# Kernel optimization log

Hardware: AMD Instinct MI355X
Metric: run time of the kernel (lower is better)

## Reference

```python
import jax, jax.numpy as jnp
import numpy as np


def setup_inputs() -> dict:
    key = jax.random.key(0)
    k1, k2, k3 = jax.random.split(key, 3)
    B, S, D_IN, D_OUT = 4, 2048, 4096, 4096
    x = jax.random.normal(k1, (B, S, D_IN), dtype=jnp.float32)
    weight = jax.random.normal(k2, (D_OUT, D_IN), dtype=jnp.float32) * 0.02
    bias = jax.random.normal(k3, (D_OUT,), dtype=jnp.float32) * 0.02
    return {"x": x, "weight": weight, "bias": bias}


def reference(x, weight, bias):
    # Column L1 norms over the output dim (torch.norm(w, p=1, dim=0)) -> [in_features]
    column_norms = jnp.abs(weight).sum(axis=0)
    q = jnp.quantile(column_norms, jnp.array([0.05, 0.95], dtype=column_norms.dtype))
    lower, upper = q[0], q[1]
    # NOTE: mask naming follows the source; 'outlier_columns' is actually the middle band.
    outlier_columns = (column_norms > lower) & (column_norms < upper)  # [in]
    binarized = ~outlier_columns  # columns that get rescaled (mask is inverted in source)

    # Row-wise abs-mean over the 'binarized' columns, detached. Shape [out, 1].
    n_bin = binarized.sum().astype(weight.dtype)
    scale = (jnp.abs(weight) * binarized[None, :]).sum(axis=-1, keepdims=True) / n_bin
    scale = jax.lax.stop_gradient(scale)

    # The STE sign assignment in the source is overwritten by w * scale, so the
    # effective binarized-column value is weight * scale (not sign(weight) * scale).
    w_bin = jnp.where(binarized[None, :], weight * scale, weight)  # [out, in]

    # F.linear(x, w_bin, bias)
    out = jnp.einsum('bsd,od->bso', x, w_bin) + bias
    return out
```

## Files before the change

kernel.cpp:

```cpp
#include <hip/hip_runtime.h>
#include <hip/hip_bf16.h>

typedef unsigned short u16;
typedef __bf16 bf16x8 __attribute__((ext_vector_type(8)));
typedef float f32x4 __attribute__((ext_vector_type(4)));
typedef __attribute__((address_space(1))) void* gp1_t;
typedef __attribute__((address_space(3))) void* lp3_t;

#define D_IN   4096
#define D_OUT  4096
#define M_ROWS 8192

#define OFF_NORMS  0u
#define OFF_QVALS  16384u
#define OFF_XB     573696u
#define OFF_WB     67682560u

static __device__ __forceinline__ u16 f2bf(float f) {
    __hip_bfloat16 h = __float2bfloat16(f);
    u16 u; __builtin_memcpy(&u, &h, 2);
    return u;
}

__global__ __launch_bounds__(256) void k1_cast_colnorm(const float* __restrict__ x,
                                                       const float* __restrict__ W,
                                                       u16* __restrict__ xb,
                                                       float* __restrict__ norms) {
    const int b = blockIdx.x;
    if (b < 512) {
        const int j  = (b & 15) * 256 + threadIdx.x;
        const int r0 = (b >> 4) * 128;
        float s = 0.f;
        #pragma unroll 4
        for (int r = 0; r < 128; ++r) s += fabsf(W[(size_t)(r0 + r) * D_IN + j]);
        atomicAdd(&norms[j], s);
    } else {
        const size_t i4 = (size_t)(b - 512) * 256 + threadIdx.x;
        const float4 v = ((const float4*)x)[i4];
        ushort4 r;
        r.x = f2bf(v.x); r.y = f2bf(v.y); r.z = f2bf(v.z); r.w = f2bf(v.w);
        ((ushort4*)xb)[i4] = r;
    }
}

__global__ void rank_select(const float* __restrict__ norms, float* __restrict__ qvals) {
    __shared__ float sn[D_IN];
    const int tid = threadIdx.x;
    for (int i = tid; i < D_IN; i += 256) sn[i] = norms[i];
    __syncthreads();
    const int j = blockIdx.x * 256 + tid;
    const float vj = sn[j];
    int r = 0;
    #pragma unroll 8
    for (int i = 0; i < D_IN; ++i) {
        const float vi = sn[i];
        r += (vi < vj) || (vi == vj && i < j);
    }
    if      (r == 204)  qvals[0] = vj;
    else if (r == 205)  qvals[1] = vj;
    else if (r == 3890) qvals[2] = vj;
    else if (r == 3891) qvals[3] = vj;
}

__global__ __launch_bounds__(256) void k3_scale_wbin(const float* __restrict__ W,
                                                     const float* __restrict__ norms,
                                                     const float* __restrict__ qvals,
                                                     u16* __restrict__ wb) {
    __shared__ float red[8];
    const int o = blockIdx.x, t = threadIdx.x;
    const int wave = t >> 6, lane = t & 63;
    const float lower = qvals[0] + 0.75f * (qvals[1] - qvals[0]);
    const float upper = qvals[2] + 0.25f * (qvals[3] - qvals[2]);
    const float4* row4 = (const float4*)(W + (size_t)o * D_IN);
    const float4* n4   = (const float4*)norms;

    float4 wv[4];
    int binbits[4];
    float cnt = 0.f, sum = 0.f;
    #pragma unroll
    for (int it = 0; it < 4; ++it) {
        const int c = it * 256 + t;
        wv[it] = row4[c];
        const float4 nv = n4[c];
        const bool b0 = !(nv.x > lower && nv.x < upper);
        const bool b1 = !(nv.y > lower && nv.y < upper);
        const bool b2 = !(nv.z > lower && nv.z < upper);
        const bool b3 = !(nv.w > lower && nv.w < upper);
        binbits[it] = (b0 ? 1 : 0) | (b1 ? 2 : 0) | (b2 ? 4 : 0) | (b3 ? 8 : 0);
        cnt += (float)(b0 + b1 + b2 + b3);
        sum += (b0 ? fabsf(wv[it].x) : 0.f) + (b1 ? fabsf(wv[it].y) : 0.f)
             + (b2 ? fabsf(wv[it].z) : 0.f) + (b3 ? fabsf(wv[it].w) : 0.f);
    }
    #pragma unroll
    for (int off = 32; off > 0; off >>= 1) {
        cnt += __shfl_down(cnt, off, 64);
        sum += __shfl_down(sum, off, 64);
    }
    if (lane == 0) { red[wave] = cnt; red[4 + wave] = sum; }
    __syncthreads();
    const float nbin = red[0] + red[1] + red[2] + red[3];
    const float ssum = red[4] + red[5] + red[6] + red[7];
    const float sc = ssum / nbin;

    ushort4* out = (ushort4*)(wb + (size_t)o * D_IN);
    #pragma unroll
    for (int it = 0; it < 4; ++it) {
        const int c = it * 256 + t;
        const int bb = binbits[it];
        ushort4 r;
        r.x = f2bf((bb & 1) ? wv[it].x * sc : wv[it].x);
        r.y = f2bf((bb & 2) ? wv[it].y * sc : wv[it].y);
        r.z = f2bf((bb & 4) ? wv[it].z * sc : wv[it].z);
        r.w = f2bf((bb & 8) ? wv[it].w * sc : wv[it].w);
        out[c] = r;
    }
}


#define BAR() do { asm volatile("" ::: "memory"); __builtin_amdgcn_s_barrier(); \
                   asm volatile("" ::: "memory"); } while (0)

#define LDA(buf, kh, mf) \
    (*(const bf16x8*)(smA + (buf)*32768 + (kh)*16384 + wr*8192 + (mf)*1024 + lane_rd))
#define LDB(buf, kh, nf) \
    (*(const bf16x8*)(smB + (buf)*32768 + (kh)*16384 + wc*4096 + (nf)*1024 + lane_rd))

#define STAGE_A(buf, kh, t) do { \
    char* l_ = smA + (buf)*32768 + (kh)*16384 + wofs; \
    __builtin_amdgcn_global_load_lds((gp1_t)(srcA0 + (t)*128 + (kh)*64), (lp3_t)l_, 16, 0, 0); \
    __builtin_amdgcn_global_load_lds((gp1_t)(srcA1 + (t)*128 + (kh)*64), (lp3_t)(l_ + 8192), 16, 0, 0); \
} while (0)

#define STAGE_B(buf, kh, t) do { \
    char* l_ = smB + (buf)*32768 + (kh)*16384 + wofs; \
    __builtin_amdgcn_global_load_lds((gp1_t)(srcB0 + (t)*128 + (kh)*64), (lp3_t)l_, 16, 0, 0); \
    __builtin_amdgcn_global_load_lds((gp1_t)(srcB1 + (t)*128 + (kh)*64), (lp3_t)(l_ + 8192), 16, 0, 0); \
} while (0)

#define MFMA __builtin_amdgcn_mfma_f32_16x16x32_bf16

#define PHASE(buf, kh, mg, RB, ST, VM) do { \
    bf16x8 a0_, a1_, a2_, a3_; \
    if (RB) { \
        bfr0 = LDB(buf, kh, 0); bfr1 = LDB(buf, kh, 1); \
        bfr2 = LDB(buf, kh, 2); bfr3 = LDB(buf, kh, 3); \
    } \
    a0_ = LDA(buf, kh, (mg)*4 + 0); \
    a1_ = LDA(buf, kh, (mg)*4 + 1); \
    a2_ = LDA(buf, kh, (mg)*4 + 2); \
    a3_ = LDA(buf, kh, (mg)*4 + 3); \
    ST; \
    if (VM) { asm volatile("s_waitcnt vmcnt(4)" ::: "memory"); } \
    BAR(); \
    asm volatile("s_waitcnt lgkmcnt(0)" ::: "memory"); \
    __builtin_amdgcn_sched_barrier(0); \
    __builtin_amdgcn_s_setprio(1); \
    acc[(mg)*4+0][0] = MFMA(a0_, bfr0, acc[(mg)*4+0][0], 0, 0, 0); \
    acc[(mg)*4+0][1] = MFMA(a0_, bfr1, acc[(mg)*4+0][1], 0, 0, 0); \
    acc[(mg)*4+0][2] = MFMA(a0_, bfr2, acc[(mg)*4+0][2], 0, 0, 0); \
    acc[(mg)*4+0][3] = MFMA(a0_, bfr3, acc[(mg)*4+0][3], 0, 0, 0); \
    acc[(mg)*4+1][0] = MFMA(a1_, bfr0, acc[(mg)*4+1][0], 0, 0, 0); \
    acc[(mg)*4+1][1] = MFMA(a1_, bfr1, acc[(mg)*4+1][1], 0, 0, 0); \
    acc[(mg)*4+1][2] = MFMA(a1_, bfr2, acc[(mg)*4+1][2], 0, 0, 0); \
    acc[(mg)*4+1][3] = MFMA(a1_, bfr3, acc[(mg)*4+1][3], 0, 0, 0); \
    acc[(mg)*4+2][0] = MFMA(a2_, bfr0, acc[(mg)*4+2][0], 0, 0, 0); \
    acc[(mg)*4+2][1] = MFMA(a2_, bfr1, acc[(mg)*4+2][1], 0, 0, 0); \
    acc[(mg)*4+2][2] = MFMA(a2_, bfr2, acc[(mg)*4+2][2], 0, 0, 0); \
    acc[(mg)*4+2][3] = MFMA(a2_, bfr3, acc[(mg)*4+2][3], 0, 0, 0); \
    acc[(mg)*4+3][0] = MFMA(a3_, bfr0, acc[(mg)*4+3][0], 0, 0, 0); \
    acc[(mg)*4+3][1] = MFMA(a3_, bfr1, acc[(mg)*4+3][1], 0, 0, 0); \
    acc[(mg)*4+3][2] = MFMA(a3_, bfr2, acc[(mg)*4+3][2], 0, 0, 0); \
    acc[(mg)*4+3][3] = MFMA(a3_, bfr3, acc[(mg)*4+3][3], 0, 0, 0); \
    __builtin_amdgcn_s_setprio(0); \
    BAR(); \
} while (0)

__global__ __launch_bounds__(512, 2) void gemm8(const u16* __restrict__ A, const u16* __restrict__ B,
                                                const float* __restrict__ bias, float* __restrict__ C) {
    __shared__ u16 sA[2][2][256 * 32];
    __shared__ u16 sB[2][2][256 * 32];
    char* const smA = (char*)&sA[0][0][0];
    char* const smB = (char*)&sB[0][0][0];

    const int tid  = threadIdx.x;
    const int wave = tid >> 6, lane = tid & 63;
    const int wr = wave >> 2, wc = wave & 3;
    const int r15 = lane & 15, q = lane >> 4;
    const int wofs = wave * 1024;

    const int swz = ((int)blockIdx.x & 7) * 64 + ((int)blockIdx.x >> 3);
    const int by = swz >> 4, bx = swz & 15;
    const int m0 = by * 256, n0 = bx * 256;

    const int lane_rd = (r15 * 64 + q * 16) ^ (((r15 >> 1) & 7) << 4);

    const int P0  = wofs + lane * 16;
    const int xv  = ((lane >> 3) & 7) << 4;
    const int lb0 = P0 ^ xv;
    const int lb1 = (P0 + 8192) ^ xv;
    const char* const gA = (const char*)(A + (size_t)m0 * D_IN);
    const char* const gB = (const char*)(B + (size_t)n0 * D_IN);
    const char* const srcA0 = gA + (size_t)(lb0 >> 6) * (D_IN * 2) + (lb0 & 63);
    const char* const srcA1 = gA + (size_t)(lb1 >> 6) * (D_IN * 2) + (lb1 & 63);
    const char* const srcB0 = gB + (size_t)(lb0 >> 6) * (D_IN * 2) + (lb0 & 63);
    const char* const srcB1 = gB + (size_t)(lb1 >> 6) * (D_IN * 2) + (lb1 & 63);

    f32x4 acc[8][4] = {};
    bf16x8 bfr0{}, bfr1{}, bfr2{}, bfr3{};

    STAGE_A(0, 0, 0); STAGE_B(0, 0, 0);
    STAGE_A(0, 1, 0); STAGE_B(0, 1, 0);
    STAGE_A(1, 0, 1); STAGE_B(1, 0, 1);
    asm volatile("s_waitcnt vmcnt(4)" ::: "memory");
    BAR();

    for (int i = 0; i < 32; ++i) {
        const int t1 = 2 * i + 1;
        const int t2 = (2 * i + 2 > 63) ? 63 : 2 * i + 2;
        const int t3 = (2 * i + 3 > 63) ? 63 : 2 * i + 3;
        PHASE(0, 0, 0, 1, STAGE_A(1, 1, t1), 0);
        PHASE(0, 0, 1, 0, STAGE_B(1, 1, t1), 0);
        PHASE(0, 1, 0, 1, STAGE_A(0, 0, t2), 0);
        PHASE(0, 1, 1, 0, STAGE_B(0, 0, t2), 1);
        PHASE(1, 0, 0, 1, STAGE_A(0, 1, t2), 0);
        PHASE(1, 0, 1, 0, STAGE_B(0, 1, t2), 0);
        PHASE(1, 1, 0, 1, STAGE_A(1, 0, t3), 0);
        PHASE(1, 1, 1, 0, STAGE_B(1, 0, t3), 1);
    }

    const int cm = q * 4;
    #pragma unroll
    for (int nf = 0; nf < 4; ++nf) {
        const int n = n0 + wc * 64 + nf * 16 + r15;
        const float bv = bias[n];
        #pragma unroll
        for (int mf = 0; mf < 8; ++mf) {
            const int mbase = m0 + wr * 128 + mf * 16 + cm;
            #pragma unroll
            for (int rr = 0; rr < 4; ++rr)
                C[(size_t)(mbase + rr) * D_OUT + n] = acc[mf][nf][rr] + bv;
        }
    }
    asm volatile("s_waitcnt vmcnt(0)" ::: "memory");
}

extern "C" void kernel_launch(void* const* d_in, const int* in_sizes, int n_in,
                              void* d_out, int out_size, void* d_ws, size_t ws_size,
                              hipStream_t stream) {
    const float* x    = (const float*)d_in[0];
    const float* W    = (const float*)d_in[1];
    const float* bias = (const float*)d_in[2];
    float* out = (float*)d_out;

    char* ws = (char*)d_ws;
    float* norms = (float*)(ws + OFF_NORMS);
    float* qvals = (float*)(ws + OFF_QVALS);
    u16*   xb    = (u16*)(ws + OFF_XB);
    u16*   wb    = (u16*)(ws + OFF_WB);

    hipMemsetAsync(norms, 0, D_IN * sizeof(float), stream);
    k1_cast_colnorm<<<512 + 32768, 256, 0, stream>>>(x, W, xb, norms);
    rank_select<<<16, 256, 0, stream>>>(norms, qvals);
    k3_scale_wbin<<<4096, 256, 0, stream>>>(W, norms, qvals, wb);
    gemm8<<<dim3(512), dim3(512), 0, stream>>>(xb, wb, bias, out);
}
```

Before: 647.9 us.

## Software-pipeline LDS fragment reads one phase ahead of MFMAs

```diff
diff --git a/kernel.cpp b/kernel.cpp
--- a/kernel.cpp
+++ b/kernel.cpp
@@ -125,52 +125,60 @@
 #define LDB(buf, kh, nf) \
     (*(const bf16x8*)(smB + (buf)*32768 + (kh)*16384 + wc*4096 + (nf)*1024 + lane_rd))
 
-#define STAGE_A(buf, kh, t) do { \
+#define STAGE_A(buf, kh, OFFV) do { \
     char* l_ = smA + (buf)*32768 + (kh)*16384 + wofs; \
-    __builtin_amdgcn_global_load_lds((gp1_t)(srcA0 + (t)*128 + (kh)*64), (lp3_t)l_, 16, 0, 0); \
-    __builtin_amdgcn_global_load_lds((gp1_t)(srcA1 + (t)*128 + (kh)*64), (lp3_t)(l_ + 8192), 16, 0, 0); \
-} while (0)
-
-#define STAGE_B(buf, kh, t) do { \
+    __builtin_amdgcn_global_load_lds((gp1_t)(srcA0 + (OFFV)), (lp3_t)l_, 16, 0, 0); \
+    __builtin_amdgcn_global_load_lds((gp1_t)(srcA1 + (OFFV)), (lp3_t)(l_ + 8192), 16, 0, 0); \
+} while (0)
+
+#define STAGE_B(buf, kh, OFFV) do { \
     char* l_ = smB + (buf)*32768 + (kh)*16384 + wofs; \
-    __builtin_amdgcn_global_load_lds((gp1_t)(srcB0 + (t)*128 + (kh)*64), (lp3_t)l_, 16, 0, 0); \
-    __builtin_amdgcn_global_load_lds((gp1_t)(srcB1 + (t)*128 + (kh)*64), (lp3_t)(l_ + 8192), 16, 0, 0); \
-} while (0)
+    __builtin_amdgcn_global_load_lds((gp1_t)(srcB0 + (OFFV)), (lp3_t)l_, 16, 0, 0); \
+    __builtin_amdgcn_global_load_lds((gp1_t)(srcB1 + (OFFV)), (lp3_t)(l_ + 8192), 16, 0, 0); \
+} while (0)
+
+#define NOST ((void)0)
+
+#define PF_A(R0,R1,R2,R3, buf, kh, mg) do { \
+    R0 = LDA(buf, kh, (mg)*4 + 0); R1 = LDA(buf, kh, (mg)*4 + 1); \
+    R2 = LDA(buf, kh, (mg)*4 + 2); R3 = LDA(buf, kh, (mg)*4 + 3); \
+} while (0)
+
+#define PF_B(R0,R1,R2,R3, buf, kh) do { \
+    R0 = LDB(buf, kh, 0); R1 = LDB(buf, kh, 1); \
+    R2 = LDB(buf, kh, 2); R3 = LDB(buf, kh, 3); \
+} while (0)
+
+#define PF_NONE ((void)0)
 
 #define MFMA __builtin_amdgcn_mfma_f32_16x16x32_bf16
 
-#define PHASE(buf, kh, mg, RB, ST, VM) do { \
-    bf16x8 a0_, a1_, a2_, a3_; \
-    if (RB) { \
-        bfr0 = LDB(buf, kh, 0); bfr1 = LDB(buf, kh, 1); \
-        bfr2 = LDB(buf, kh, 2); bfr3 = LDB(buf, kh, 3); \
-    } \
-    a0_ = LDA(buf, kh, (mg)*4 + 0); \
-    a1_ = LDA(buf, kh, (mg)*4 + 1); \
-    a2_ = LDA(buf, kh, (mg)*4 + 2); \
-    a3_ = LDA(buf, kh, (mg)*4 + 3); \
+#define PHASE(mg, A0_,A1_,A2_,A3_, B0_,B1_,B2_,B3_, VM, ST, PFA, PFB) do { \
     ST; \
-    if (VM) { asm volatile("s_waitcnt vmcnt(4)" ::: "memory"); } \
+    if ((VM) == 1) { asm volatile("s_waitcnt vmcnt(4)" ::: "memory"); } \
     BAR(); \
     asm volatile("s_waitcnt lgkmcnt(0)" ::: "memory"); \
     __builtin_amdgcn_sched_barrier(0); \
     __builtin_amdgcn_s_setprio(1); \
-    acc[(mg)*4+0][0] = MFMA(a0_, bfr0, acc[(mg)*4+0][0], 0, 0, 0); \
-    acc[(mg)*4+0][1] = MFMA(a0_, bfr1, acc[(mg)*4+0][1], 0, 0, 0); \
-    acc[(mg)*4+0][2] = MFMA(a0_, bfr2, acc[(mg)*4+0][2], 0, 0, 0); \
-    acc[(mg)*4+0][3] = MFMA(a0_, bfr3, acc[(mg)*4+0][3], 0, 0, 0); \
-    acc[(mg)*4+1][0] = MFMA(a1_, bfr0, acc[(mg)*4+1][0], 0, 0, 0); \
-    acc[(mg)*4+1][1] = MFMA(a1_, bfr1, acc[(mg)*4+1][1], 0, 0, 0); \
-    acc[(mg)*4+1][2] = MFMA(a1_, bfr2, acc[(mg)*4+1][2], 0, 0, 0); \
-    acc[(mg)*4+1][3] = MFMA(a1_, bfr3, acc[(mg)*4+1][3], 0, 0, 0); \
-    acc[(mg)*4+2][0] = MFMA(a2_, bfr0, acc[(mg)*4+2][0], 0, 0, 0); \
-    acc[(mg)*4+2][1] = MFMA(a2_, bfr1, acc[(mg)*4+2][1], 0, 0, 0); \
-    acc[(mg)*4+2][2] = MFMA(a2_, bfr2, acc[(mg)*4+2][2], 0, 0, 0); \
-    acc[(mg)*4+2][3] = MFMA(a2_, bfr3, acc[(mg)*4+2][3], 0, 0, 0); \
-    acc[(mg)*4+3][0] = MFMA(a3_, bfr0, acc[(mg)*4+3][0], 0, 0, 0); \
-    acc[(mg)*4+3][1] = MFMA(a3_, bfr1, acc[(mg)*4+3][1], 0, 0, 0); \
-    acc[(mg)*4+3][2] = MFMA(a3_, bfr2, acc[(mg)*4+3][2], 0, 0, 0); \
-    acc[(mg)*4+3][3] = MFMA(a3_, bfr3, acc[(mg)*4+3][3], 0, 0, 0); \
+    PFA; \
+    PFB; \
+    __builtin_amdgcn_sched_barrier(0); \
+    acc[(mg)*4+0][0] = MFMA(A0_, B0_, acc[(mg)*4+0][0], 0, 0, 0); \
+    acc[(mg)*4+0][1] = MFMA(A0_, B1_, acc[(mg)*4+0][1], 0, 0, 0); \
+    acc[(mg)*4+0][2] = MFMA(A0_, B2_, acc[(mg)*4+0][2], 0, 0, 0); \
+    acc[(mg)*4+0][3] = MFMA(A0_, B3_, acc[(mg)*4+0][3], 0, 0, 0); \
+    acc[(mg)*4+1][0] = MFMA(A1_, B0_, acc[(mg)*4+1][0], 0, 0, 0); \
+    acc[(mg)*4+1][1] = MFMA(A1_, B1_, acc[(mg)*4+1][1], 0, 0, 0); \
+    acc[(mg)*4+1][2] = MFMA(A1_, B2_, acc[(mg)*4+1][2], 0, 0, 0); \
+    acc[(mg)*4+1][3] = MFMA(A1_, B3_, acc[(mg)*4+1][3], 0, 0, 0); \
+    acc[(mg)*4+2][0] = MFMA(A2_, B0_, acc[(mg)*4+2][0], 0, 0, 0); \
+    acc[(mg)*4+2][1] = MFMA(A2_, B1_, acc[(mg)*4+2][1], 0, 0, 0); \
+    acc[(mg)*4+2][2] = MFMA(A2_, B2_, acc[(mg)*4+2][2], 0, 0, 0); \
+    acc[(mg)*4+2][3] = MFMA(A2_, B3_, acc[(mg)*4+2][3], 0, 0, 0); \
+    acc[(mg)*4+3][0] = MFMA(A3_, B0_, acc[(mg)*4+3][0], 0, 0, 0); \
+    acc[(mg)*4+3][1] = MFMA(A3_, B1_, acc[(mg)*4+3][1], 0, 0, 0); \
+    acc[(mg)*4+3][2] = MFMA(A3_, B2_, acc[(mg)*4+3][2], 0, 0, 0); \
+    acc[(mg)*4+3][3] = MFMA(A3_, B3_, acc[(mg)*4+3][3], 0, 0, 0); \
     __builtin_amdgcn_s_setprio(0); \
     BAR(); \
 } while (0)
@@ -206,26 +214,33 @@
     const char* const srcB1 = gB + (size_t)(lb1 >> 6) * (D_IN * 2) + (lb1 & 63);
 
     f32x4 acc[8][4] = {};
-    bf16x8 bfr0{}, bfr1{}, bfr2{}, bfr3{};
-
-    STAGE_A(0, 0, 0); STAGE_B(0, 0, 0);
-    STAGE_A(0, 1, 0); STAGE_B(0, 1, 0);
-    STAGE_A(1, 0, 1); STAGE_B(1, 0, 1);
+    bf16x8 aX0{}, aX1{}, aX2{}, aX3{}, aY0{}, aY1{}, aY2{}, aY3{};
+    bf16x8 b00{}, b01{}, b02{}, b03{}, b10{}, b11{}, b12{}, b13{};
+
+    STAGE_A(0, 0, 0);   STAGE_B(0, 0, 0);
+    STAGE_A(0, 1, 64);  STAGE_B(0, 1, 64);
+    STAGE_A(1, 0, 128); STAGE_B(1, 0, 128);
     asm volatile("s_waitcnt vmcnt(4)" ::: "memory");
     BAR();
-
+    PF_A(aX0, aX1, aX2, aX3, 0, 0, 0);
+    PF_B(b00, b01, b02, b03, 0, 0);
+
+    #pragma unroll 1
     for (int i = 0; i < 32; ++i) {
-        const int t1 = 2 * i + 1;
-        const int t2 = (2 * i + 2 > 63) ? 63 : 2 * i + 2;
-        const int t3 = (2 * i + 3 > 63) ? 63 : 2 * i + 3;
-        PHASE(0, 0, 0, 1, STAGE_A(1, 1, t1), 0);
-        PHASE(0, 0, 1, 0, STAGE_B(1, 1, t1), 0);
-        PHASE(0, 1, 0, 1, STAGE_A(0, 0, t2), 0);
-        PHASE(0, 1, 1, 0, STAGE_B(0, 0, t2), 1);
-        PHASE(1, 0, 0, 1, STAGE_A(0, 1, t2), 0);
-        PHASE(1, 0, 1, 0, STAGE_B(0, 1, t2), 0);
-        PHASE(1, 1, 0, 1, STAGE_A(1, 0, t3), 0);
-        PHASE(1, 1, 1, 0, STAGE_B(1, 0, t3), 1);
+        const int t2  = (2 * i + 2 > 63) ? 63 : 2 * i + 2;
+        const int t3  = (2 * i + 3 > 63) ? 63 : 2 * i + 3;
+        const int o11 = i * 256 + 192;
+        const int o00 = t2 * 128;
+        const int o01 = o00 + 64;
+        const int o10 = t3 * 128;
+        PHASE(0, aX0,aX1,aX2,aX3, b00,b01,b02,b03, 0, STAGE_A(1,1,o11), PF_A(aY0,aY1,aY2,aY3, 0,0,1), PF_NONE);
+        PHASE(1, aY0,aY1,aY2,aY3, b00,b01,b02,b03, 0, STAGE_B(1,1,o11), PF_A(aX0,aX1,aX2,aX3, 0,1,0), PF_B(b10,b11,b12,b13, 0,1));
+        PHASE(0, aX0,aX1,aX2,aX3, b10,b11,b12,b13, 0, STAGE_A(0,0,o00), PF_A(aY0,aY1,aY2,aY3, 0,1,1), PF_NONE);
+        PHASE(1, aY0,aY1,aY2,aY3, b10,b11,b12,b13, 1, STAGE_B(0,0,o00), PF_A(aX0,aX1,aX2,aX3, 1,0,0), PF_B(b00,b01,b02,b03, 1,0));
+        PHASE(0, aX0,aX1,aX2,aX3, b00,b01,b02,b03, 0, STAGE_A(0,1,o01), PF_A(aY0,aY1,aY2,aY3, 1,0,1), PF_NONE);
+        PHASE(1, aY0,aY1,aY2,aY3, b00,b01,b02,b03, 0, STAGE_B(0,1,o01), PF_A(aX0,aX1,aX2,aX3, 1,1,0), PF_B(b10,b11,b12,b13, 1,1));
+        PHASE(0, aX0,aX1,aX2,aX3, b10,b11,b12,b13, 0, STAGE_A(1,0,o10), PF_A(aY0,aY1,aY2,aY3, 1,1,1), PF_NONE);
+        PHASE(1, aY0,aY1,aY2,aY3, b10,b11,b12,b13, 1, STAGE_B(1,0,o10), PF_A(aX0,aX1,aX2,aX3, 0,0,0), PF_B(b00,b01,b02,b03, 0,0));
     }
 
     const int cm = q * 4;
```

Result: no change. 652.5 us (+0.7%).
